# Kernel tuning notes

Measured on AMD Instinct MI355X. Metric: run time of the kernel, lower is better.

The kernel has to match this reference:

```python
import jax, jax.numpy as jnp
import numpy as np

SMOOTH = 1.0
ALPHA = 1.0
GAMMA = 2.0
W_CE, W_DICE, W_JACCARD, W_FOCAL = 1.0, 1.0, 1.0, 1.0


def setup_inputs() -> dict:
    key = jax.random.key(0)
    k1, k2 = jax.random.split(key)
    pred = jax.random.normal(k1, (8, 21, 512, 512), dtype=jnp.float32)
    target = jax.random.randint(k2, (8, 512, 512), 0, 21, dtype=jnp.int32)
    return {"pred": pred, "target": target}


def _combo_loss(pred, target):
    B, C = pred.shape[0], pred.shape[1]
    # softmax / log-softmax over class axis (dim=1)
    logp = jax.nn.log_softmax(pred, axis=1)            # [B,C,H,W]
    probs = jnp.exp(logp)                              # [B,C,H,W]
    oh = jax.nn.one_hot(target, C, axis=1, dtype=pred.dtype)  # [B,C,H,W]

    # per-(batch, class) sums shared by Dice and Jaccard
    inter = jnp.sum(probs * oh, axis=(2, 3))           # [B,C]
    psum = jnp.sum(probs, axis=(2, 3))                 # [B,C]
    tsum = jnp.sum(oh, axis=(2, 3))                    # [B,C]

    # Dice: sum over classes of per-batch dice, then 1 - mean/C
    dice = jnp.sum((2.0 * inter + SMOOTH) / (psum + tsum + SMOOTH), axis=1)  # [B]
    dice_loss = 1.0 - jnp.mean(dice) / C

    # Jaccard
    jac = jnp.sum((inter + SMOOTH) / (psum + tsum - inter + SMOOTH), axis=1)  # [B]
    jaccard_loss = 1.0 - jnp.mean(jac) / C

    # per-pixel cross entropy: -log p[target]
    ce_pix = -jnp.take_along_axis(logp, target[:, None].astype(jnp.int32), axis=1)[:, 0]  # [B,H,W]
    ce_loss = jnp.mean(ce_pix)

    # focal
    pt = jnp.exp(-ce_pix)
    focal_loss = jnp.mean(ALPHA * (1.0 - pt) ** GAMMA * ce_pix)

    return (W_CE * ce_loss + W_DICE * dice_loss
            + W_JACCARD * jaccard_loss + W_FOCAL * focal_loss)


def reference(pred, target):
    return _combo_loss(pred, target)
```

## Files before the change

### kernel.cpp

```cpp
#include <hip/hip_runtime.h>
#include <math.h>

constexpr int B = 8, C = 21, H = 512, W = 512;
constexpr int HW = H * W;
constexpr int THREADS = 256;
constexpr int NITER = 2;
constexpr int PIX_PER_BLOCK = THREADS * 4 * NITER;
constexpr int BLOCKS_PER_BATCH = HW / PIX_PER_BLOCK;
constexpr int NBLOCKS = B * BLOCKS_PER_BATCH;

constexpr int WS_PSUM = 0;
constexpr int WS_INTER = B * C;
constexpr int WS_TSUM = 2 * B * C;
constexpr int WS_CE = 3 * B * C;
constexpr int WS_FOC = 3 * B * C + NBLOCKS;

__global__ __launch_bounds__(512) void zero_accum(float* ws) {
    int i = threadIdx.x;
    if (i < 3 * B * C) ws[i] = 0.0f;
}

__global__ __launch_bounds__(THREADS) void combo_main(
        const float* __restrict__ pred, const int* __restrict__ tgt,
        float* __restrict__ ws) {
    __shared__ float s_psum[C], s_inter[C], s_tsum[C];
    __shared__ float s_ce, s_foc;
    const int tid = threadIdx.x;
    if (tid < C) {
        s_psum[tid] = 0.0f;
        s_inter[tid] = 0.0f;
        s_tsum[tid] = 0.0f;
    }
    if (tid == 0) { s_ce = 0.0f; s_foc = 0.0f; }
    __syncthreads();

    const int bid = blockIdx.x;
    const int b = bid / BLOCKS_PER_BATCH;
    const int chunk = bid % BLOCKS_PER_BATCH;
    const float* base = pred + (size_t)b * C * HW + (size_t)chunk * PIX_PER_BLOCK;
    const int* tbase = tgt + (size_t)b * HW + (size_t)chunk * PIX_PER_BLOCK;

    float r[C];
#pragma unroll
    for (int c = 0; c < C; ++c) r[c] = 0.0f;
    float ce_acc = 0.0f, foc_acc = 0.0f;

    for (int it = 0; it < NITER; ++it) {
        const int off = it * THREADS * 4 + tid * 4;
        const float4* p4 = (const float4*)(base + off);
        const int4 tg = *(const int4*)(tbase + off);

        float4 s4 = make_float4(0.f, 0.f, 0.f, 0.f);
        float4 xt = make_float4(0.f, 0.f, 0.f, 0.f);
        unsigned xp0[C], xp1[C];

#pragma unroll
        for (int c = 0; c < C; ++c) {
            float4 x = p4[(size_t)c * (HW / 4)];
            unsigned pa, pb;
            asm("v_cvt_pk_bf16_f32 %0, %1, %2" : "=v"(pa) : "v"(x.x), "v"(x.y));
            asm("v_cvt_pk_bf16_f32 %0, %1, %2" : "=v"(pb) : "v"(x.z), "v"(x.w));
            xp0[c] = pa; xp1[c] = pb;
            s4.x += __expf(x.x);
            s4.y += __expf(x.y);
            s4.z += __expf(x.z);
            s4.w += __expf(x.w);
            if (tg.x == c) xt.x = x.x;
            if (tg.y == c) xt.y = x.y;
            if (tg.z == c) xt.z = x.z;
            if (tg.w == c) xt.w = x.w;
        }

        float4 lns;
        lns.x = __logf(s4.x); lns.y = __logf(s4.y);
        lns.z = __logf(s4.z); lns.w = __logf(s4.w);

        float ce0 = lns.x - xt.x, ce1 = lns.y - xt.y;
        float ce2 = lns.z - xt.z, ce3 = lns.w - xt.w;
        float pt0 = __expf(-ce0), pt1 = __expf(-ce1);
        float pt2 = __expf(-ce2), pt3 = __expf(-ce3);
        float om0 = 1.f - pt0, om1 = 1.f - pt1, om2 = 1.f - pt2, om3 = 1.f - pt3;
        ce_acc += ce0 + ce1 + ce2 + ce3;
        foc_acc += om0 * om0 * ce0 + om1 * om1 * ce1 +
                   om2 * om2 * ce2 + om3 * om3 * ce3;

        atomicAdd(&s_inter[tg.x], pt0);
        atomicAdd(&s_inter[tg.y], pt1);
        atomicAdd(&s_inter[tg.z], pt2);
        atomicAdd(&s_inter[tg.w], pt3);
        atomicAdd(&s_tsum[tg.x], 1.0f);
        atomicAdd(&s_tsum[tg.y], 1.0f);
        atomicAdd(&s_tsum[tg.z], 1.0f);
        atomicAdd(&s_tsum[tg.w], 1.0f);

#pragma unroll
        for (int c = 0; c < C; ++c) {
            float x0 = __uint_as_float(xp0[c] << 16);
            float x1 = __uint_as_float(xp0[c] & 0xffff0000u);
            float x2 = __uint_as_float(xp1[c] << 16);
            float x3 = __uint_as_float(xp1[c] & 0xffff0000u);
            r[c] += __expf(x0 - lns.x) + __expf(x1 - lns.y) +
                    __expf(x2 - lns.z) + __expf(x3 - lns.w);
        }
    }

    const int lane = tid & 63;
#pragma unroll
    for (int c = 0; c < C; ++c) {
        float v = r[c];
#pragma unroll
        for (int o = 32; o; o >>= 1) v += __shfl_xor(v, o, 64);
        if (lane == 0) atomicAdd(&s_psum[c], v);
    }
    {
        float v = ce_acc, f = foc_acc;
#pragma unroll
        for (int o = 32; o; o >>= 1) {
            v += __shfl_xor(v, o, 64);
            f += __shfl_xor(f, o, 64);
        }
        if (lane == 0) { atomicAdd(&s_ce, v); atomicAdd(&s_foc, f); }
    }
    __syncthreads();

    if (tid < C) {
        atomicAdd(&ws[WS_PSUM + b * C + tid], s_psum[tid]);
        atomicAdd(&ws[WS_INTER + b * C + tid], s_inter[tid]);
        atomicAdd(&ws[WS_TSUM + b * C + tid], s_tsum[tid]);
    }
    if (tid == 0) {
        ws[WS_CE + bid] = s_ce;
        ws[WS_FOC + bid] = s_foc;
    }
}

__global__ __launch_bounds__(THREADS) void combo_final(
        const float* __restrict__ ws, float* __restrict__ out) {
    __shared__ float s_ce, s_foc, s_dj, s_jj;
    if (threadIdx.x == 0) { s_ce = 0.f; s_foc = 0.f; s_dj = 0.f; s_jj = 0.f; }
    __syncthreads();

    const int tid = threadIdx.x;
    float ce = 0.f, fo = 0.f;
    for (int i = tid; i < NBLOCKS; i += THREADS) {
        ce += ws[WS_CE + i];
        fo += ws[WS_FOC + i];
    }
    float dj = 0.f, jj = 0.f;
    for (int i = tid; i < B * C; i += THREADS) {
        float it = ws[WS_INTER + i], ps = ws[WS_PSUM + i], ts = ws[WS_TSUM + i];
        dj += (2.0f * it + 1.0f) / (ps + ts + 1.0f);
        jj += (it + 1.0f) / (ps + ts - it + 1.0f);
    }
    const int lane = tid & 63;
#pragma unroll
    for (int o = 32; o; o >>= 1) {
        ce += __shfl_xor(ce, o, 64);
        fo += __shfl_xor(fo, o, 64);
        dj += __shfl_xor(dj, o, 64);
        jj += __shfl_xor(jj, o, 64);
    }
    if (lane == 0) {
        atomicAdd(&s_ce, ce);
        atomicAdd(&s_foc, fo);
        atomicAdd(&s_dj, dj);
        atomicAdd(&s_jj, jj);
    }
    __syncthreads();
    if (tid == 0) {
        const float N = (float)B * (float)HW;
        out[0] = s_ce / N + s_foc / N +
                 (1.0f - s_dj / (float)(B * C)) +
                 (1.0f - s_jj / (float)(B * C));
    }
}

extern "C" void kernel_launch(void* const* d_in, const int* in_sizes, int n_in,
                              void* d_out, int out_size, void* d_ws, size_t ws_size,
                              hipStream_t stream) {
    const float* pred = (const float*)d_in[0];
    const int* tgt = (const int*)d_in[1];
    float* ws = (float*)d_ws;
    float* out = (float*)d_out;

    zero_accum<<<1, 512, 0, stream>>>(ws);
    combo_main<<<NBLOCKS, THREADS, 0, stream>>>(pred, tgt, ws);
    combo_final<<<1, THREADS, 0, stream>>>(ws, out);
}
```

Baseline: 58.42 us.

## Stage logits in LDS via global_load_lds with single-wave blocks

Switches to one-wavefront blocks that load each class row directly from global into LDS with global_load_lds, stores exp(x) back into the LDS tile, and computes softmax probabilities as exp times reciprocal sum instead of a second exp on bf16-packed logits. Per-class psum is reduced in registers and written straight to global atomics, which drops the shared-memory psum and CE/focal atomics. This removes register pressure from the packed copies and the second round of exps, but it quadruples the block count and the global atomic traffic, and each iteration waits for all its loads to finish before computing, with no overlap.

Measured after the change: 95.83 us. 1.64x slower.

```diff
diff --git a/kernel.cpp b/kernel.cpp
--- a/kernel.cpp
+++ b/kernel.cpp
@@ -3,9 +3,11 @@
 
 constexpr int B = 8, C = 21, H = 512, W = 512;
 constexpr int HW = H * W;
-constexpr int THREADS = 256;
+constexpr int THREADS = 64;
+constexpr int PPT = 4;
 constexpr int NITER = 2;
-constexpr int PIX_PER_BLOCK = THREADS * 4 * NITER;
+constexpr int PIX_PER_TILE = THREADS * PPT;
+constexpr int PIX_PER_BLOCK = PIX_PER_TILE * NITER;
 constexpr int BLOCKS_PER_BATCH = HW / PIX_PER_BLOCK;
 constexpr int NBLOCKS = B * BLOCKS_PER_BATCH;
 
@@ -15,6 +17,9 @@
 constexpr int WS_CE = 3 * B * C;
 constexpr int WS_FOC = 3 * B * C + NBLOCKS;
 
+typedef __attribute__((address_space(3))) unsigned lds_u32;
+typedef const __attribute__((address_space(1))) unsigned g_u32;
+
 __global__ __launch_bounds__(512) void zero_accum(float* ws) {
     int i = threadIdx.x;
     if (i < 3 * B * C) ws[i] = 0.0f;
@@ -23,22 +28,16 @@
 __global__ __launch_bounds__(THREADS) void combo_main(
         const float* __restrict__ pred, const int* __restrict__ tgt,
         float* __restrict__ ws) {
-    __shared__ float s_psum[C], s_inter[C], s_tsum[C];
-    __shared__ float s_ce, s_foc;
-    const int tid = threadIdx.x;
-    if (tid < C) {
-        s_psum[tid] = 0.0f;
-        s_inter[tid] = 0.0f;
-        s_tsum[tid] = 0.0f;
-    }
-    if (tid == 0) { s_ce = 0.0f; s_foc = 0.0f; }
+    __shared__ float tile[C][PIX_PER_TILE];
+    __shared__ float s_inter[C], s_tsum[C];
+
+    const int lane = threadIdx.x;
+    if (lane < C) { s_inter[lane] = 0.0f; s_tsum[lane] = 0.0f; }
     __syncthreads();
 
     const int bid = blockIdx.x;
     const int b = bid / BLOCKS_PER_BATCH;
-    const int chunk = bid % BLOCKS_PER_BATCH;
-    const float* base = pred + (size_t)b * C * HW + (size_t)chunk * PIX_PER_BLOCK;
-    const int* tbase = tgt + (size_t)b * HW + (size_t)chunk * PIX_PER_BLOCK;
+    const int chunk = bid - b * BLOCKS_PER_BATCH;
 
     float r[C];
 #pragma unroll
@@ -46,29 +45,32 @@
     float ce_acc = 0.0f, foc_acc = 0.0f;
 
     for (int it = 0; it < NITER; ++it) {
-        const int off = it * THREADS * 4 + tid * 4;
-        const float4* p4 = (const float4*)(base + off);
-        const int4 tg = *(const int4*)(tbase + off);
+        const int pix0 = chunk * PIX_PER_BLOCK + it * PIX_PER_TILE;
+
+        const int4 tg = *(const int4*)(tgt + (size_t)b * HW + pix0 + lane * PPT);
+
+        const float* gbase = pred + (size_t)b * C * HW + pix0 + lane * PPT;
+#pragma unroll
+        for (int c = 0; c < C; ++c) {
+            __builtin_amdgcn_global_load_lds((g_u32*)(gbase + (size_t)c * HW),
+                                             (lds_u32*)&tile[c][0], 16, 0, 0);
+        }
+        asm volatile("s_waitcnt vmcnt(0)" ::: "memory");
 
         float4 s4 = make_float4(0.f, 0.f, 0.f, 0.f);
         float4 xt = make_float4(0.f, 0.f, 0.f, 0.f);
-        unsigned xp0[C], xp1[C];
-
 #pragma unroll
         for (int c = 0; c < C; ++c) {
-            float4 x = p4[(size_t)c * (HW / 4)];
-            unsigned pa, pb;
-            asm("v_cvt_pk_bf16_f32 %0, %1, %2" : "=v"(pa) : "v"(x.x), "v"(x.y));
-            asm("v_cvt_pk_bf16_f32 %0, %1, %2" : "=v"(pb) : "v"(x.z), "v"(x.w));
-            xp0[c] = pa; xp1[c] = pb;
-            s4.x += __expf(x.x);
-            s4.y += __expf(x.y);
-            s4.z += __expf(x.z);
-            s4.w += __expf(x.w);
-            if (tg.x == c) xt.x = x.x;
-            if (tg.y == c) xt.y = x.y;
-            if (tg.z == c) xt.z = x.z;
-            if (tg.w == c) xt.w = x.w;
+            float4 x = *(const float4*)&tile[c][lane * PPT];
+            float4 e;
+            e.x = __expf(x.x); e.y = __expf(x.y);
+            e.z = __expf(x.z); e.w = __expf(x.w);
+            xt.x = (tg.x == c) ? x.x : xt.x;
+            xt.y = (tg.y == c) ? x.y : xt.y;
+            xt.z = (tg.z == c) ? x.z : xt.z;
+            xt.w = (tg.w == c) ? x.w : xt.w;
+            s4.x += e.x; s4.y += e.y; s4.z += e.z; s4.w += e.w;
+            *(float4*)&tile[c][lane * PPT] = e;
         }
 
         float4 lns;
@@ -93,48 +95,47 @@
         atomicAdd(&s_tsum[tg.z], 1.0f);
         atomicAdd(&s_tsum[tg.w], 1.0f);
 
+        float4 inv;
+        inv.x = __builtin_amdgcn_rcpf(s4.x);
+        inv.y = __builtin_amdgcn_rcpf(s4.y);
+        inv.z = __builtin_amdgcn_rcpf(s4.z);
+        inv.w = __builtin_amdgcn_rcpf(s4.w);
 #pragma unroll
         for (int c = 0; c < C; ++c) {
-            float x0 = __uint_as_float(xp0[c] << 16);
-            float x1 = __uint_as_float(xp0[c] & 0xffff0000u);
-            float x2 = __uint_as_float(xp1[c] << 16);
-            float x3 = __uint_as_float(xp1[c] & 0xffff0000u);
-            r[c] += __expf(x0 - lns.x) + __expf(x1 - lns.y) +
-                    __expf(x2 - lns.z) + __expf(x3 - lns.w);
+            float4 e = *(const float4*)&tile[c][lane * PPT];
+            r[c] += e.x * inv.x + e.y * inv.y + e.z * inv.z + e.w * inv.w;
         }
     }
 
-    const int lane = tid & 63;
+    float rmine = 0.0f;
 #pragma unroll
     for (int c = 0; c < C; ++c) {
         float v = r[c];
 #pragma unroll
         for (int o = 32; o; o >>= 1) v += __shfl_xor(v, o, 64);
-        if (lane == 0) atomicAdd(&s_psum[c], v);
+        rmine = (lane == c) ? v : rmine;
     }
     {
-        float v = ce_acc, f = foc_acc;
 #pragma unroll
         for (int o = 32; o; o >>= 1) {
-            v += __shfl_xor(v, o, 64);
-            f += __shfl_xor(f, o, 64);
+            ce_acc += __shfl_xor(ce_acc, o, 64);
+            foc_acc += __shfl_xor(foc_acc, o, 64);
         }
-        if (lane == 0) { atomicAdd(&s_ce, v); atomicAdd(&s_foc, f); }
     }
     __syncthreads();
 
-    if (tid < C) {
-        atomicAdd(&ws[WS_PSUM + b * C + tid], s_psum[tid]);
-        atomicAdd(&ws[WS_INTER + b * C + tid], s_inter[tid]);
-        atomicAdd(&ws[WS_TSUM + b * C + tid], s_tsum[tid]);
+    if (lane < C) {
+        atomicAdd(&ws[WS_PSUM + b * C + lane], rmine);
+        atomicAdd(&ws[WS_INTER + b * C + lane], s_inter[lane]);
+        atomicAdd(&ws[WS_TSUM + b * C + lane], s_tsum[lane]);
     }
-    if (tid == 0) {
-        ws[WS_CE + bid] = s_ce;
-        ws[WS_FOC + bid] = s_foc;
+    if (lane == 0) {
+        ws[WS_CE + bid] = ce_acc;
+        ws[WS_FOC + bid] = foc_acc;
     }
 }
 
-__global__ __launch_bounds__(THREADS) void combo_final(
+__global__ __launch_bounds__(256) void combo_final(
         const float* __restrict__ ws, float* __restrict__ out) {
     __shared__ float s_ce, s_foc, s_dj, s_jj;
     if (threadIdx.x == 0) { s_ce = 0.f; s_foc = 0.f; s_dj = 0.f; s_jj = 0.f; }
@@ -142,12 +143,12 @@
 
     const int tid = threadIdx.x;
     float ce = 0.f, fo = 0.f;
-    for (int i = tid; i < NBLOCKS; i += THREADS) {
+    for (int i = tid; i < NBLOCKS; i += 256) {
         ce += ws[WS_CE + i];
         fo += ws[WS_FOC + i];
     }
     float dj = 0.f, jj = 0.f;
-    for (int i = tid; i < B * C; i += THREADS) {
+    for (int i = tid; i < B * C; i += 256) {
         float it = ws[WS_INTER + i], ps = ws[WS_PSUM + i], ts = ws[WS_TSUM + i];
         dj += (2.0f * it + 1.0f) / (ps + ts + 1.0f);
         jj += (it + 1.0f) / (ps + ts - it + 1.0f);
@@ -185,5 +186,5 @@
 
     zero_accum<<<1, 512, 0, stream>>>(ws);
     combo_main<<<NBLOCKS, THREADS, 0, stream>>>(pred, tgt, ws);
-    combo_final<<<1, THREADS, 0, stream>>>(ws, out);
+    combo_final<<<1, 256, 0, stream>>>(ws, out);
 }
```
